# Performance work log

Measured on AMD Instinct MI355X. Metric: run time of the kernel, lower is better.

## Reference

```python
import jax, jax.numpy as jnp
import numpy as np

TAU = 2.0      # LIF membrane time constant
K = 2          # MaxPool1d kernel/stride
ALPHA = 4.0    # spikingjelly surrogate.Sigmoid default alpha
EPS = 1e-5     # BatchNorm1d eps
VTH = 1.0      # LIF v_threshold default

@jax.custom_vjp
def spike(x):
    # Heaviside forward, sigmoid surrogate gradient (spikingjelly surrogate.Sigmoid)
    return (x >= 0.0).astype(x.dtype)

def _spike_fwd(x):
    return spike(x), x

def _spike_bwd(x, g):
    s = jax.nn.sigmoid(ALPHA * x)
    return (g * ALPHA * s * (1.0 - s),)

spike.defvjp(_spike_fwd, _spike_bwd)


def setup_inputs() -> dict:
    key = jax.random.key(0)
    k1, k2 = jax.random.split(key)
    T, B, N, D, O = 4, 32, 1024, 512, 512
    x = jax.random.normal(k1, (T, B, N, D), jnp.float32)
    W = jax.random.normal(k2, (O, D), jnp.float32) * 0.02
    gamma = jnp.ones((O,), jnp.float32)
    beta = jnp.zeros((O,), jnp.float32)
    running_mean = jnp.zeros((O,), jnp.float32)
    running_var = jnp.ones((O,), jnp.float32)
    return {"x": x, "W": W, "gamma": gamma, "beta": beta,
            "running_mean": running_mean, "running_var": running_var}


def reference(x, W, gamma, beta, running_mean, running_var):
    T, B, N, D = x.shape
    O = W.shape[0]
    # Linear (no bias): [T,B,N,D] x [O,D] -> [T,B,N,O]
    h = jnp.einsum('tbnd,od->tbno', x, W)
    # BatchNorm1d in inference form (running stats), fused affine
    inv = gamma * jax.lax.rsqrt(running_var + EPS)
    h = h * inv + (beta - running_mean * inv)
    # MaxPool1d(kernel_size=K, stride=K) over feature dim -> [T,B,N,O//K]
    h = h.reshape(T, B, N, O // K, K).max(axis=-1)
    # Multi-step LIF: v = v + (x - v)/tau; spike = H(v - vth); hard reset to 0
    def step(v, xt):
        v = v + (xt - v) / TAU
        s = spike(v - VTH)
        v = v * (1.0 - jax.lax.stop_gradient(s))  # detach_reset=True
        return v, s
    _, spikes = jax.lax.scan(step, jnp.zeros_like(h[0]), h)
    return spikes
```

## Files before the change

### kernel.cpp

```cpp
#include <hip/hip_runtime.h>

constexpr int T_ = 4, B_ = 32, N_ = 1024, D_ = 512, O_ = 512, OP_ = 256;
constexpr int M_ = T_ * B_ * N_;
constexpr unsigned CAP = 1u * 1024 * 1024;

constexpr size_t WS_CNT  = 0;
constexpr size_t WS_WP   = 1u << 20;
constexpr size_t WS_LIST = WS_WP + (1u << 20);
constexpr size_t WS_NEED = WS_LIST + (size_t)CAP * 4;

constexpr int RSTRIDE = 72;
constexpr int BUFSZ   = 128 * RSTRIDE;

typedef __attribute__((ext_vector_type(8)))  short bf8;
typedef __attribute__((ext_vector_type(16))) float f16v;

union U2B { struct { uint2 a, b; } p; bf8 v; };

__device__ __forceinline__ unsigned cvtpk(float x0, float x1) {
    unsigned r;
    asm("v_cvt_pk_bf16_f32 %0, %1, %2" : "=v"(r) : "v"(x0), "v"(x1));
    return r;
}
__device__ __forceinline__ float hi_lo_f(unsigned u) { return __uint_as_float(u << 16); }
__device__ __forceinline__ float hi_hi_f(unsigned u) { return __uint_as_float(u & 0xffff0000u); }

__global__ __launch_bounds__(256) void k_wprep(const float* __restrict__ W,
                                               unsigned short* __restrict__ wp,
                                               unsigned* __restrict__ cnt)
{
    if (blockIdx.x == 0 && threadIdx.x == 0) *cnt = 0u;
    const int c = blockIdx.x * 256 + threadIdx.x;
    const int lane = c & 63, q = (c >> 6) & 7, j = (c >> 9) & 15, panel = c >> 13;
    const int colblk = panel >> 1, half = panel & 1;
    const int tm = q >> 2, eo = (q >> 1) & 1, Kh = q & 1;
    const int col = colblk * 128 + half * 64 + 2 * (lane & 31) + eo;
    const int k0 = j * 32 + Kh * 16 + (lane >> 5) * 8;
    const float* src = W + (size_t)col * 512 + k0;
    const float4 v0 = *(const float4*)(src);
    const float4 v1 = *(const float4*)(src + 4);
    const float xs[8] = {v0.x, v0.y, v0.z, v0.w, v1.x, v1.y, v1.z, v1.w};
    unsigned o[4];
    #pragma unroll
    for (int p = 0; p < 4; ++p) {
        const unsigned hi = cvtpk(xs[2 * p], xs[2 * p + 1]);
        if (tm == 0) {
            o[p] = hi;
        } else {
            const float l0 = xs[2 * p] - hi_lo_f(hi);
            const float l1 = xs[2 * p + 1] - hi_hi_f(hi);
            o[p] = cvtpk(l0, l1);
        }
    }
    *(uint4*)(wp + (size_t)c * 8) = make_uint4(o[0], o[1], o[2], o[3]);
}

__global__ __launch_bounds__(256, 3) void k_gemm(
    const float* __restrict__ x, const unsigned short* __restrict__ wp,
    const float* __restrict__ gamma, const float* __restrict__ beta,
    const float* __restrict__ rmean, const float* __restrict__ rvar,
    float* __restrict__ out, unsigned* __restrict__ cnt, unsigned* __restrict__ list)
{
    extern __shared__ char lds[];
    const int tid  = threadIdx.x;
    const int lane = tid & 63;
    const int wid  = tid >> 6;

    const int dd = blockIdx.x;
    const int w  = (dd & 7) * 512 + (dd >> 3);
    const int colblk = w & 3, rowblk = w >> 2;
    const int c0  = colblk * 128;
    const int wr0 = (wid >> 1) * 64, wc0 = (wid & 1) * 64;

    const int cE = c0 + wc0 + 2 * (lane & 31);
    const int cO = cE + 1;
    const float invE = gamma[cE] / sqrtf(rvar[cE] + 1e-5f);
    const float addE = beta[cE] - rmean[cE] * invE;
    const float invO = gamma[cO] / sqrtf(rvar[cO] + 1e-5f);
    const float addO = beta[cO] - rmean[cO] * invO;
    asm volatile("s_waitcnt vmcnt(0)" ::: "memory");
    __builtin_amdgcn_sched_barrier(0);

    const int arow = tid >> 1;
    const int kh   = tid & 1;
    const int t_a  = arow & 3;
    const int sl_a = arow >> 2;
    const unsigned vA = (unsigned)(t_a * 32768 + rowblk * 32 + sl_a) * 2048u
                      + (unsigned)kh * 64u;
    const int wA0 = arow * RSTRIDE + kh * 32;

    int rA00, rA01, rA10, rA11;
    {
        const int qv = lane & 31, hs = lane >> 5;
        const int r0 = wr0 + qv, r1 = wr0 + 32 + qv;
        rA00 = r0 * RSTRIDE + 0  + hs * 16;
        rA01 = r0 * RSTRIDE + 32 + hs * 16;
        rA10 = r1 * RSTRIDE + 0  + hs * 16;
        rA11 = r1 * RSTRIDE + 32 + hs * 16;
    }

    const int panel = colblk * 2 + (wid & 1);
    const unsigned vBb = ((unsigned)panel << 17) + (unsigned)lane * 16u;

    f16v accE[2], accO[2];
    #pragma unroll
    for (int i = 0; i < 2; ++i) { accE[i] = (f16v)0.0f; accO[i] = (f16v)0.0f; }

    float4 Aa[4], Ab[4];
    bf8 Bf[8];
    bf8 ah[4];

#define SCHED __builtin_amdgcn_sched_barrier(0)

#define ALOAD(AI, K)                                                              \
    do {                                                                          \
        asm volatile("global_load_dwordx4 %0, %1, %2 offset:%3"                   \
                     : "=v"(AI[0]) : "v"(vA), "s"(x), "n"((K)*128 + 0)  : "memory"); \
        asm volatile("global_load_dwordx4 %0, %1, %2 offset:%3"                   \
                     : "=v"(AI[1]) : "v"(vA), "s"(x), "n"((K)*128 + 16) : "memory"); \
        asm volatile("global_load_dwordx4 %0, %1, %2 offset:%3"                   \
                     : "=v"(AI[2]) : "v"(vA), "s"(x), "n"((K)*128 + 32) : "memory"); \
        asm volatile("global_load_dwordx4 %0, %1, %2 offset:%3"                   \
                     : "=v"(AI[3]) : "v"(vA), "s"(x), "n"((K)*128 + 48) : "memory"); \
    } while (0)

#define BGRP(KH, K)                                                               \
    do {                                                                          \
        const unsigned vk  = vBb + (unsigned)((K) * 8192 + (KH) * 1024);          \
        const unsigned vk2 = vk + 4096u;                                          \
        asm volatile("global_load_dwordx4 %0, %1, %2 offset:%3"                   \
                     : "=v"(Bf[(KH)*4 + 0]) : "v"(vk),  "s"(wp), "n"(0)    : "memory"); \
        asm volatile("global_load_dwordx4 %0, %1, %2 offset:%3"                   \
                     : "=v"(Bf[(KH)*4 + 1]) : "v"(vk),  "s"(wp), "n"(2048) : "memory"); \
        asm volatile("global_load_dwordx4 %0, %1, %2 offset:%3"                   \
                     : "=v"(Bf[(KH)*4 + 2]) : "v"(vk2), "s"(wp), "n"(0)    : "memory"); \
        asm volatile("global_load_dwordx4 %0, %1, %2 offset:%3"                   \
                     : "=v"(Bf[(KH)*4 + 3]) : "v"(vk2), "s"(wp), "n"(2048) : "memory"); \
    } while (0)

#define DSR1(J, IDX, RA)                                                          \
    do {                                                                          \
        const char* bR = lds + ((J) & 1) * BUFSZ;                                 \
        U2B t;                                                                    \
        t.p.a = *(const uint2*)(bR + (RA));                                       \
        t.p.b = *(const uint2*)(bR + (RA) + 8);                                   \
        ah[IDX] = t.v;                                                            \
    } while (0)

#define CONVW(AC, BUF)                                                            \
    do {                                                                          \
        char* pw = lds + (BUF) * BUFSZ + wA0;                                     \
        const unsigned q0 = cvtpk(AC[0].x, AC[0].y), q1 = cvtpk(AC[0].z, AC[0].w);\
        const unsigned q2 = cvtpk(AC[1].x, AC[1].y), q3 = cvtpk(AC[1].z, AC[1].w);\
        *(uint2*)(pw + 0)  = make_uint2(q0, q1);                                  \
        *(uint2*)(pw + 8)  = make_uint2(q2, q3);                                  \
        const unsigned q4 = cvtpk(AC[2].x, AC[2].y), q5 = cvtpk(AC[2].z, AC[2].w);\
        const unsigned q6 = cvtpk(AC[3].x, AC[3].y), q7 = cvtpk(AC[3].z, AC[3].w);\
        *(uint2*)(pw + 16) = make_uint2(q4, q5);                                  \
        *(uint2*)(pw + 24) = make_uint2(q6, q7);                                  \
    } while (0)

#define MGRP4(KH, RT)                                                             \
    do {                                                                          \
        accE[RT] = __builtin_amdgcn_mfma_f32_32x32x16_bf16(ah[(RT)*2+(KH)], Bf[(KH)*4+0], accE[RT], 0, 0, 0); \
        accO[RT] = __builtin_amdgcn_mfma_f32_32x32x16_bf16(ah[(RT)*2+(KH)], Bf[(KH)*4+1], accO[RT], 0, 0, 0); \
        accE[RT] = __builtin_amdgcn_mfma_f32_32x32x16_bf16(ah[(RT)*2+(KH)], Bf[(KH)*4+2], accE[RT], 0, 0, 0); \
        accO[RT] = __builtin_amdgcn_mfma_f32_32x32x16_bf16(ah[(RT)*2+(KH)], Bf[(KH)*4+3], accO[RT], 0, 0, 0); \
    } while (0)

#define PRIO1 __builtin_amdgcn_s_setprio(1)
#define PRIO0 __builtin_amdgcn_s_setprio(0)

#define ITER(J, ATGT, ACV)                                                        \
    do {                                                                          \
        SCHED;                                                                    \
        asm volatile("s_waitcnt vmcnt(8)" ::: "memory");        \
        asm volatile("s_waitcnt lgkmcnt(0)" ::: "memory");      \
        __builtin_amdgcn_s_barrier();                                             \
        SCHED;                                                                    \
        DSR1(J, 0, rA00);                                       \
        SCHED;                                                                    \
        asm volatile("s_waitcnt vmcnt(4)" ::: "memory");       \
        SCHED;                                                                    \
        PRIO1; MGRP4(0, 0); PRIO0;                                                \
        SCHED;                                                                    \
        DSR1(J, 2, rA10);                                       \
        if ((J) + 2 <= 15) { ALOAD(ATGT, (J) + 2); }                              \
        SCHED;                                                                    \
        PRIO1; MGRP4(0, 1); PRIO0;                                                \
        SCHED;                                                                    \
        DSR1(J, 1, rA01);                                       \
        DSR1(J, 3, rA11);                                       \
        BGRP(0, (J) + 1);                                                         \
        SCHED;                                                                    \
        asm volatile("s_waitcnt vmcnt(8)" ::: "memory");       \
        SCHED;                                                                    \
        PRIO1; MGRP4(1, 0); PRIO0;                                                \
        SCHED;                                                                    \
        CONVW(ACV, ((J) + 1) & 1);                             \
        SCHED;                                                                    \
        PRIO1; MGRP4(1, 1); PRIO0;                                                \
        SCHED;                                                                    \
        BGRP(1, (J) + 1);                                                         \
        SCHED;                                                                    \
    } while (0)

    SCHED;
    ALOAD(Aa, 0);
    ALOAD(Ab, 1);
    SCHED;
    BGRP(0, 0);
    BGRP(1, 0);
    SCHED;
    asm volatile("s_waitcnt vmcnt(12)" ::: "memory");
    SCHED;
    CONVW(Aa, 0);
    SCHED;

    ITER(0,  Aa, Ab);
    ITER(1,  Ab, Aa);
    ITER(2,  Aa, Ab);
    ITER(3,  Ab, Aa);
    ITER(4,  Aa, Ab);
    ITER(5,  Ab, Aa);
    ITER(6,  Aa, Ab);
    ITER(7,  Ab, Aa);
    ITER(8,  Aa, Ab);
    ITER(9,  Ab, Aa);
    ITER(10, Aa, Ab);
    ITER(11, Ab, Aa);
    ITER(12, Aa, Ab);
    ITER(13, Ab, Aa);

    SCHED;
    asm volatile("s_waitcnt vmcnt(8)" ::: "memory");
    asm volatile("s_waitcnt lgkmcnt(0)" ::: "memory");
    __builtin_amdgcn_s_barrier();
    SCHED;
    DSR1(14, 0, rA00);
    SCHED;
    asm volatile("s_waitcnt vmcnt(4)" ::: "memory");
    SCHED;
    PRIO1; MGRP4(0, 0); PRIO0;
    SCHED;
    DSR1(14, 2, rA10);
    SCHED;
    PRIO1; MGRP4(0, 1); PRIO0;
    SCHED;
    DSR1(14, 1, rA01);
    DSR1(14, 3, rA11);
    BGRP(0, 15);
    SCHED;
    asm volatile("s_waitcnt vmcnt(4)" ::: "memory");
    SCHED;
    PRIO1; MGRP4(1, 0); PRIO0;
    SCHED;
    CONVW(Ab, 1);
    SCHED;
    PRIO1; MGRP4(1, 1); PRIO0;
    SCHED;
    BGRP(1, 15);
    SCHED;

    asm volatile("s_waitcnt lgkmcnt(0)" ::: "memory");
    __builtin_amdgcn_s_barrier();
    SCHED;
    DSR1(15, 0, rA00);
    DSR1(15, 2, rA10);
    SCHED;
    asm volatile("s_waitcnt vmcnt(4)" ::: "memory");
    SCHED;
    PRIO1; MGRP4(0, 0); PRIO0;
    SCHED;
    DSR1(15, 1, rA01);
    DSR1(15, 3, rA11);
    SCHED;
    PRIO1; MGRP4(0, 1); PRIO0;
    SCHED;
    asm volatile("s_waitcnt vmcnt(0)" ::: "memory");
    SCHED;
    PRIO1; MGRP4(1, 0); PRIO0;
    SCHED;
    PRIO1; MGRP4(1, 1); PRIO0;
    SCHED;

#undef ITER
#undef PRIO1
#undef PRIO0
#undef MGRP4
#undef DSR1
#undef CONVW
#undef BGRP
#undef ALOAD
#undef SCHED

    const int opL = ((c0 + wc0) >> 1) + (lane & 31);
    #pragma unroll
    for (int rt = 0; rt < 2; ++rt) {
        #pragma unroll
        for (int g = 0; g < 4; ++g) {
            const int site = rowblk * 32 + (wid >> 1) * 16 + rt * 8 + 2 * g + (lane >> 5);
            const int bI = site >> 10, nI = site & 1023;
            float v = 0.0f;
            bool flg = false;
            #pragma unroll
            for (int t = 0; t < 4; ++t) {
                const float hE = accE[rt][g * 4 + t] * invE + addE;
                const float hO = accO[rt][g * 4 + t] * invO + addO;
                const float m = fmaxf(hE, hO);
                v = (v + m) * 0.5f;
                const float dv = v - 1.0f;
                const bool sp = dv >= 0.0f;
                out[(((size_t)t * 32 + bI) * 1024 + nI) * 256 + opL] = sp ? 1.0f : 0.0f;
                flg |= (fabsf(dv) < 1e-2f);
                if (sp) v = 0.0f;
            }
            if (flg) {
                unsigned idx = atomicAdd(cnt, 1u);
                if (idx < CAP) list[idx] = ((unsigned)site << 8) | (unsigned)opL;
            }
        }
    }
}

__global__ __launch_bounds__(256) void k_repair(
    const float* __restrict__ x, const float* __restrict__ W,
    const float* __restrict__ gamma, const float* __restrict__ beta,
    const float* __restrict__ rmean, const float* __restrict__ rvar,
    float* __restrict__ out, const unsigned* __restrict__ cnt,
    const unsigned* __restrict__ list)
{
    unsigned count = *cnt;
    if (count > CAP) count = CAP;
    const int lane = threadIdx.x & 63;
    const unsigned gw = (blockIdx.x * 256u + threadIdx.x) >> 6;
    const unsigned nw = (gridDim.x * 256u) >> 6;
    const int d0 = lane * 8;

    for (unsigned j = gw; j < count; j += nw) {
        const unsigned e = list[j];
        const int op = e & 255;
        const int site = e >> 8;
        const int bI = site >> 10, nI = site & 1023;

        double wv[2][8];
        #pragma unroll
        for (int p = 0; p < 2; ++p) {
            const float* Wr = W + (size_t)(2 * op + p) * D_ + d0;
            const float4 a = *(const float4*)(Wr);
            const float4 b = *(const float4*)(Wr + 4);
            wv[p][0] = a.x; wv[p][1] = a.y; wv[p][2] = a.z; wv[p][3] = a.w;
            wv[p][4] = b.x; wv[p][5] = b.y; wv[p][6] = b.z; wv[p][7] = b.w;
        }

        double h[4][2];
        #pragma unroll
        for (int t = 0; t < 4; ++t) {
            const float* xr = x + (((size_t)t * 32 + bI) * 1024 + nI) * D_ + d0;
            const float4 a = *(const float4*)(xr);
            const float4 b = *(const float4*)(xr + 4);
            const double xv[8] = {(double)a.x, (double)a.y, (double)a.z, (double)a.w,
                                  (double)b.x, (double)b.y, (double)b.z, (double)b.w};
            #pragma unroll
            for (int p = 0; p < 2; ++p) {
                double s0 = 0, s1 = 0, s2 = 0, s3 = 0;
                s0 = fma(xv[0], wv[p][0], s0); s1 = fma(xv[1], wv[p][1], s1);
                s2 = fma(xv[2], wv[p][2], s2); s3 = fma(xv[3], wv[p][3], s3);
                s0 = fma(xv[4], wv[p][4], s0); s1 = fma(xv[5], wv[p][5], s1);
                s2 = fma(xv[6], wv[p][6], s2); s3 = fma(xv[7], wv[p][7], s3);
                double s = (s0 + s1) + (s2 + s3);
                #pragma unroll
                for (int off = 32; off > 0; off >>= 1)
                    s += __shfl_xor(s, off, 64);
                h[t][p] = s;
            }
        }

        double iv[2], ad[2];
        #pragma unroll
        for (int p = 0; p < 2; ++p) {
            const int c = 2 * op + p;
            iv[p] = (double)gamma[c] / sqrt((double)rvar[c] + 1e-5);
            ad[p] = (double)beta[c] - (double)rmean[c] * iv[p];
        }
        double v = 0.0;
        #pragma unroll
        for (int t = 0; t < 4; ++t) {
            const double h0 = h[t][0] * iv[0] + ad[0];
            const double h1 = h[t][1] * iv[1] + ad[1];
            const double m = fmax(h0, h1);
            v = (v + m) * 0.5;
            const bool sp = (v >= 1.0);
            if (lane == t)
                out[(((size_t)t * 32 + bI) * 1024 + nI) * 256 + op] = sp ? 1.0f : 0.0f;
            if (sp) v = 0.0;
        }
    }
}

constexpr int FB_SITES = 32, FB_ROWS = 128, FB_BN = 64, FB_BK = 16;

__global__ __launch_bounds__(256)
void snn_fused_f64(const float* __restrict__ x, const float* __restrict__ W,
                   const float* __restrict__ gamma, const float* __restrict__ beta,
                   const float* __restrict__ rmean, const float* __restrict__ rvar,
                   float* __restrict__ out)
{
    __shared__ float As[FB_BK][FB_ROWS];
    __shared__ float Bs[FB_BK][FB_BN];
    const int tid = threadIdx.x;
    const int tx = tid & 15, ty = tid >> 4;
    const int c0 = blockIdx.x * FB_BN;
    const int site_base = blockIdx.y * FB_SITES;
    const int b = site_base / N_, n0 = site_base % N_;
    const int lrow = tid >> 1, lk = (tid & 1) * 8;
    const int s_l = lrow >> 2, t_l = lrow & 3;
    const float* xrow = x + (size_t)((t_l * B_ + b) * N_ + (n0 + s_l)) * D_ + lk;
    const int wc = tid & 63, wk = (tid >> 6) * 4;
    const float* wrow = W + (size_t)(c0 + wc) * D_ + wk;
    double acc[8][4];
    #pragma unroll
    for (int i = 0; i < 8; ++i)
        #pragma unroll
        for (int j = 0; j < 4; ++j) acc[i][j] = 0.0;
    for (int k0 = 0; k0 < D_; k0 += FB_BK) {
        const float4 a0 = *(const float4*)(xrow + k0);
        const float4 a1 = *(const float4*)(xrow + k0 + 4);
        const float4 w4 = *(const float4*)(wrow + k0);
        As[lk + 0][lrow] = a0.x; As[lk + 1][lrow] = a0.y; As[lk + 2][lrow] = a0.z; As[lk + 3][lrow] = a0.w;
        As[lk + 4][lrow] = a1.x; As[lk + 5][lrow] = a1.y; As[lk + 6][lrow] = a1.z; As[lk + 7][lrow] = a1.w;
        Bs[wk + 0][wc] = w4.x; Bs[wk + 1][wc] = w4.y; Bs[wk + 2][wc] = w4.z; Bs[wk + 3][wc] = w4.w;
        __syncthreads();
        #pragma unroll
        for (int k = 0; k < FB_BK; ++k) {
            const float4 af0 = *(const float4*)&As[k][ty * 8];
            const float4 af1 = *(const float4*)&As[k][ty * 8 + 4];
            const float4 bf = *(const float4*)&Bs[k][tx * 4];
            const double ad[8] = {(double)af0.x, (double)af0.y, (double)af0.z, (double)af0.w,
                                  (double)af1.x, (double)af1.y, (double)af1.z, (double)af1.w};
            const double bd[4] = {(double)bf.x, (double)bf.y, (double)bf.z, (double)bf.w};
            #pragma unroll
            for (int i = 0; i < 8; ++i)
                #pragma unroll
                for (int j = 0; j < 4; ++j) acc[i][j] = fma(ad[i], bd[j], acc[i][j]);
        }
        __syncthreads();
    }
    double invd[4], addd[4];
    #pragma unroll
    for (int j = 0; j < 4; ++j) {
        const int c = c0 + tx * 4 + j;
        const double ivv = (double)gamma[c] / sqrt((double)rvar[c] + 1e-5);
        invd[j] = ivv; addd[j] = (double)beta[c] - (double)rmean[c] * ivv;
    }
    #pragma unroll
    for (int si = 0; si < 2; ++si) {
        const int n = n0 + ty * 2 + si;
        #pragma unroll
        for (int p = 0; p < 2; ++p) {
            const int op = (c0 >> 1) + tx * 2 + p;
            double v = 0.0;
            #pragma unroll
            for (int t = 0; t < 4; ++t) {
                const int i = si * 4 + t;
                const double h0 = acc[i][2 * p] * invd[2 * p] + addd[2 * p];
                const double h1 = acc[i][2 * p + 1] * invd[2 * p + 1] + addd[2 * p + 1];
                const double m = fmax(h0, h1);
                v = v + (m - v) * 0.5;
                const bool sp = (v >= 1.0);
                out[((size_t)(t * B_ + b) * N_ + n) * OP_ + op] = sp ? 1.0f : 0.0f;
                if (sp) v = 0.0;
            }
        }
    }
}

extern "C" void kernel_launch(void* const* d_in, const int* in_sizes, int n_in,
                              void* d_out, int out_size, void* d_ws, size_t ws_size,
                              hipStream_t stream)
{
    const float* x     = (const float*)d_in[0];
    const float* W     = (const float*)d_in[1];
    const float* gamma = (const float*)d_in[2];
    const float* beta  = (const float*)d_in[3];
    const float* rmean = (const float*)d_in[4];
    const float* rvar  = (const float*)d_in[5];
    float* out = (float*)d_out;

    if (ws_size < WS_NEED) {
        dim3 grid(O_ / FB_BN, (B_ * N_) / FB_SITES);
        snn_fused_f64<<<grid, dim3(256), 0, stream>>>(x, W, gamma, beta, rmean, rvar, out);
        return;
    }

    char* ws = (char*)d_ws;
    unsigned* cnt = (unsigned*)(ws + WS_CNT);
    unsigned short* wp = (unsigned short*)(ws + WS_WP);
    unsigned* list = (unsigned*)(ws + WS_LIST);

    k_wprep<<<256, 256, 0, stream>>>(W, wp, cnt);
    k_gemm<<<4096, 256, 2 * BUFSZ, stream>>>(x, wp, gamma, beta, rmean, rvar, out, cnt, list);
    k_repair<<<512, 256, 0, stream>>>(x, W, gamma, beta, rmean, rvar, out, cnt, list);
}
```

Measured before the change: 201.7 us.

## Drop split-bf16 weight residual term, halving MFMA work; widen repair band

The weight prep no longer emits a bf16 hi/lo split. The GEMM now issues half as many MFMAs and B-operand loads per k-step, using single-bf16 weights, and the inner loop schedule is restructured to match. To make up for the lost precision, the near-threshold flag band that routes outputs to the exact fp32/f64 repair kernel is widened from 1e-2 to 2.5e-2, so more sites may need repair. The aim is to cut matrix-core and weight-load cost in the main kernel, at the price of more repair work and a correctness risk if bf16-weight errors ever exceed the band.

```diff
diff --git a/kernel.cpp b/kernel.cpp
--- a/kernel.cpp
+++ b/kernel.cpp
@@ -6,7 +6,7 @@
 
 constexpr size_t WS_CNT  = 0;
 constexpr size_t WS_WP   = 1u << 20;
-constexpr size_t WS_LIST = WS_WP + (1u << 20);
+constexpr size_t WS_LIST = WS_WP + (1u << 19);
 constexpr size_t WS_NEED = WS_LIST + (size_t)CAP * 4;
 
 constexpr int RSTRIDE = 72;
@@ -22,8 +22,6 @@
     asm("v_cvt_pk_bf16_f32 %0, %1, %2" : "=v"(r) : "v"(x0), "v"(x1));
     return r;
 }
-__device__ __forceinline__ float hi_lo_f(unsigned u) { return __uint_as_float(u << 16); }
-__device__ __forceinline__ float hi_hi_f(unsigned u) { return __uint_as_float(u & 0xffff0000u); }
 
 __global__ __launch_bounds__(256) void k_wprep(const float* __restrict__ W,
                                                unsigned short* __restrict__ wp,
@@ -31,28 +29,17 @@
 {
     if (blockIdx.x == 0 && threadIdx.x == 0) *cnt = 0u;
     const int c = blockIdx.x * 256 + threadIdx.x;
-    const int lane = c & 63, q = (c >> 6) & 7, j = (c >> 9) & 15, panel = c >> 13;
+    const int lane = c & 63, q = (c >> 6) & 3, j = (c >> 8) & 15, panel = c >> 12;
     const int colblk = panel >> 1, half = panel & 1;
-    const int tm = q >> 2, eo = (q >> 1) & 1, Kh = q & 1;
+    const int eo = (q >> 1) & 1, Kh = q & 1;
     const int col = colblk * 128 + half * 64 + 2 * (lane & 31) + eo;
     const int k0 = j * 32 + Kh * 16 + (lane >> 5) * 8;
     const float* src = W + (size_t)col * 512 + k0;
     const float4 v0 = *(const float4*)(src);
     const float4 v1 = *(const float4*)(src + 4);
-    const float xs[8] = {v0.x, v0.y, v0.z, v0.w, v1.x, v1.y, v1.z, v1.w};
-    unsigned o[4];
-    #pragma unroll
-    for (int p = 0; p < 4; ++p) {
-        const unsigned hi = cvtpk(xs[2 * p], xs[2 * p + 1]);
-        if (tm == 0) {
-            o[p] = hi;
-        } else {
-            const float l0 = xs[2 * p] - hi_lo_f(hi);
-            const float l1 = xs[2 * p + 1] - hi_hi_f(hi);
-            o[p] = cvtpk(l0, l1);
-        }
-    }
-    *(uint4*)(wp + (size_t)c * 8) = make_uint4(o[0], o[1], o[2], o[3]);
+    const unsigned o0 = cvtpk(v0.x, v0.y), o1 = cvtpk(v0.z, v0.w);
+    const unsigned o2 = cvtpk(v1.x, v1.y), o3 = cvtpk(v1.z, v1.w);
+    *(uint4*)(wp + (size_t)c * 8) = make_uint4(o0, o1, o2, o3);
 }
 
 __global__ __launch_bounds__(256, 3) void k_gemm(
@@ -100,14 +87,14 @@
     }
 
     const int panel = colblk * 2 + (wid & 1);
-    const unsigned vBb = ((unsigned)panel << 17) + (unsigned)lane * 16u;
+    const unsigned vBb = ((unsigned)panel << 16) + (unsigned)lane * 16u;
 
     f16v accE[2], accO[2];
     #pragma unroll
     for (int i = 0; i < 2; ++i) { accE[i] = (f16v)0.0f; accO[i] = (f16v)0.0f; }
 
     float4 Aa[4], Ab[4];
-    bf8 Bf[8];
+    bf8 Bf[4];
     bf8 ah[4];
 
 #define SCHED __builtin_amdgcn_sched_barrier(0)
@@ -124,18 +111,15 @@
                      : "=v"(AI[3]) : "v"(vA), "s"(x), "n"((K)*128 + 48) : "memory"); \
     } while (0)
 
-#define BGRP(KH, K)                                                               \
-    do {                                                                          \
-        const unsigned vk  = vBb + (unsigned)((K) * 8192 + (KH) * 1024);          \
-        const unsigned vk2 = vk + 4096u;                                          \
-        asm volatile("global_load_dwordx4 %0, %1, %2 offset:%3"                   \
-                     : "=v"(Bf[(KH)*4 + 0]) : "v"(vk),  "s"(wp), "n"(0)    : "memory"); \
-        asm volatile("global_load_dwordx4 %0, %1, %2 offset:%3"                   \
-                     : "=v"(Bf[(KH)*4 + 1]) : "v"(vk),  "s"(wp), "n"(2048) : "memory"); \
-        asm volatile("global_load_dwordx4 %0, %1, %2 offset:%3"                   \
-                     : "=v"(Bf[(KH)*4 + 2]) : "v"(vk2), "s"(wp), "n"(0)    : "memory"); \
-        asm volatile("global_load_dwordx4 %0, %1, %2 offset:%3"                   \
-                     : "=v"(Bf[(KH)*4 + 3]) : "v"(vk2), "s"(wp), "n"(2048) : "memory"); \
+#define BGRPH(KH, K)                                                              \
+    do {                                                                          \
+        const unsigned vk = vBb + (unsigned)(K) * 4096u;                          \
+        asm volatile("global_load_dwordx4 %0, %1, %2 offset:%3"                   \
+                     : "=v"(Bf[0 + (KH)]) : "v"(vk), "s"(wp),                     \
+                       "n"((KH)*1024)        : "memory");                         \
+        asm volatile("global_load_dwordx4 %0, %1, %2 offset:%3"                   \
+                     : "=v"(Bf[2 + (KH)]) : "v"(vk), "s"(wp),                     \
+                       "n"(2048 + (KH)*1024) : "memory");                         \
     } while (0)
 
 #define DSR1(J, IDX, RA)                                                          \
@@ -160,48 +144,45 @@
         *(uint2*)(pw + 24) = make_uint2(q6, q7);                                  \
     } while (0)
 
-#define MGRP4(KH, RT)                                                             \
-    do {                                                                          \
-        accE[RT] = __builtin_amdgcn_mfma_f32_32x32x16_bf16(ah[(RT)*2+(KH)], Bf[(KH)*4+0], accE[RT], 0, 0, 0); \
-        accO[RT] = __builtin_amdgcn_mfma_f32_32x32x16_bf16(ah[(RT)*2+(KH)], Bf[(KH)*4+1], accO[RT], 0, 0, 0); \
-        accE[RT] = __builtin_amdgcn_mfma_f32_32x32x16_bf16(ah[(RT)*2+(KH)], Bf[(KH)*4+2], accE[RT], 0, 0, 0); \
-        accO[RT] = __builtin_amdgcn_mfma_f32_32x32x16_bf16(ah[(RT)*2+(KH)], Bf[(KH)*4+3], accO[RT], 0, 0, 0); \
+#define MGRP(KH)                                                                  \
+    do {                                                                          \
+        accE[0] = __builtin_amdgcn_mfma_f32_32x32x16_bf16(ah[0 + (KH)], Bf[0 + (KH)], accE[0], 0, 0, 0); \
+        accO[0] = __builtin_amdgcn_mfma_f32_32x32x16_bf16(ah[0 + (KH)], Bf[2 + (KH)], accO[0], 0, 0, 0); \
+        accE[1] = __builtin_amdgcn_mfma_f32_32x32x16_bf16(ah[2 + (KH)], Bf[0 + (KH)], accE[1], 0, 0, 0); \
+        accO[1] = __builtin_amdgcn_mfma_f32_32x32x16_bf16(ah[2 + (KH)], Bf[2 + (KH)], accO[1], 0, 0, 0); \
     } while (0)
 
 #define PRIO1 __builtin_amdgcn_s_setprio(1)
 #define PRIO0 __builtin_amdgcn_s_setprio(0)
 
-#define ITER(J, ATGT, ACV)                                                        \
-    do {                                                                          \
-        SCHED;                                                                    \
-        asm volatile("s_waitcnt vmcnt(8)" ::: "memory");        \
+#define ITER(J, ATGT, ACV, NB0, NB1)                                              \
+    do {                                                                          \
+        SCHED;                                                                    \
+        asm volatile("s_waitcnt vmcnt(4)" ::: "memory");        \
         asm volatile("s_waitcnt lgkmcnt(0)" ::: "memory");      \
         __builtin_amdgcn_s_barrier();                                             \
         SCHED;                                                                    \
-        DSR1(J, 0, rA00);                                       \
-        SCHED;                                                                    \
-        asm volatile("s_waitcnt vmcnt(4)" ::: "memory");       \
-        SCHED;                                                                    \
-        PRIO1; MGRP4(0, 0); PRIO0;                                                \
-        SCHED;                                                                    \
-        DSR1(J, 2, rA10);                                       \
+        DSR1(J, 0, rA00);                                                         \
+        DSR1(J, 1, rA01);                                                         \
+        DSR1(J, 2, rA10);                                                         \
+        DSR1(J, 3, rA11);                                                         \
+        SCHED;                                                                    \
         if ((J) + 2 <= 15) { ALOAD(ATGT, (J) + 2); }                              \
         SCHED;                                                                    \
-        PRIO1; MGRP4(0, 1); PRIO0;                                                \
-        SCHED;                                                                    \
-        DSR1(J, 1, rA01);                                       \
-        DSR1(J, 3, rA11);                                       \
-        BGRP(0, (J) + 1);                                                         \
-        SCHED;                                                                    \
-        asm volatile("s_waitcnt vmcnt(8)" ::: "memory");       \
-        SCHED;                                                                    \
-        PRIO1; MGRP4(1, 0); PRIO0;                                                \
+        asm volatile("s_waitcnt vmcnt(" NB0 ")" ::: "memory");   \
+        asm volatile("s_waitcnt lgkmcnt(0)" ::: "memory");     \
+        SCHED;                                                                    \
+        PRIO1; MGRP(0); PRIO0;                                                    \
+        SCHED;                                                                    \
+        BGRPH(0, (J) + 1);                                                        \
+        SCHED;                                                                    \
+        asm volatile("s_waitcnt vmcnt(" NB1 ")" ::: "memory");   \
+        SCHED;                                                                    \
+        PRIO1; MGRP(1); PRIO0;                                                    \
         SCHED;                                                                    \
         CONVW(ACV, ((J) + 1) & 1);                             \
         SCHED;                                                                    \
-        PRIO1; MGRP4(1, 1); PRIO0;                                                \
-        SCHED;                                                                    \
-        BGRP(1, (J) + 1);                                                         \
+        BGRPH(1, (J) + 1);                                                        \
         SCHED;                                                                    \
     } while (0)
 
@@ -209,88 +190,56 @@
     ALOAD(Aa, 0);
     ALOAD(Ab, 1);
     SCHED;
-    BGRP(0, 0);
-    BGRP(1, 0);
-    SCHED;
-    asm volatile("s_waitcnt vmcnt(12)" ::: "memory");
+    BGRPH(0, 0);
+    BGRPH(1, 0);
+    SCHED;
+    asm volatile("s_waitcnt vmcnt(8)" ::: "memory");
     SCHED;
     CONVW(Aa, 0);
     SCHED;
 
-    ITER(0,  Aa, Ab);
-    ITER(1,  Ab, Aa);
-    ITER(2,  Aa, Ab);
-    ITER(3,  Ab, Aa);
-    ITER(4,  Aa, Ab);
-    ITER(5,  Ab, Aa);
-    ITER(6,  Aa, Ab);
-    ITER(7,  Ab, Aa);
-    ITER(8,  Aa, Ab);
-    ITER(9,  Ab, Aa);
-    ITER(10, Aa, Ab);
-    ITER(11, Ab, Aa);
-    ITER(12, Aa, Ab);
-    ITER(13, Ab, Aa);
-
-    SCHED;
-    asm volatile("s_waitcnt vmcnt(8)" ::: "memory");
+    ITER(0,  Aa, Ab, "6", "6");
+    ITER(1,  Ab, Aa, "6", "6");
+    ITER(2,  Aa, Ab, "6", "6");
+    ITER(3,  Ab, Aa, "6", "6");
+    ITER(4,  Aa, Ab, "6", "6");
+    ITER(5,  Ab, Aa, "6", "6");
+    ITER(6,  Aa, Ab, "6", "6");
+    ITER(7,  Ab, Aa, "6", "6");
+    ITER(8,  Aa, Ab, "6", "6");
+    ITER(9,  Ab, Aa, "6", "6");
+    ITER(10, Aa, Ab, "6", "6");
+    ITER(11, Ab, Aa, "6", "6");
+    ITER(12, Aa, Ab, "6", "6");
+    ITER(13, Ab, Aa, "6", "6");
+    ITER(14, Aa, Ab, "2", "2");
+
+    SCHED;
     asm volatile("s_waitcnt lgkmcnt(0)" ::: "memory");
     __builtin_amdgcn_s_barrier();
     SCHED;
-    DSR1(14, 0, rA00);
-    SCHED;
-    asm volatile("s_waitcnt vmcnt(4)" ::: "memory");
-    SCHED;
-    PRIO1; MGRP4(0, 0); PRIO0;
-    SCHED;
-    DSR1(14, 2, rA10);
-    SCHED;
-    PRIO1; MGRP4(0, 1); PRIO0;
-    SCHED;
-    DSR1(14, 1, rA01);
-    DSR1(14, 3, rA11);
-    BGRP(0, 15);
-    SCHED;
-    asm volatile("s_waitcnt vmcnt(4)" ::: "memory");
-    SCHED;
-    PRIO1; MGRP4(1, 0); PRIO0;
-    SCHED;
-    CONVW(Ab, 1);
-    SCHED;
-    PRIO1; MGRP4(1, 1); PRIO0;
-    SCHED;
-    BGRP(1, 15);
-    SCHED;
-
+    DSR1(15, 0, rA00);
+    DSR1(15, 1, rA01);
+    DSR1(15, 2, rA10);
+    DSR1(15, 3, rA11);
+    SCHED;
+    asm volatile("s_waitcnt vmcnt(2)" ::: "memory");
     asm volatile("s_waitcnt lgkmcnt(0)" ::: "memory");
-    __builtin_amdgcn_s_barrier();
-    SCHED;
-    DSR1(15, 0, rA00);
-    DSR1(15, 2, rA10);
-    SCHED;
-    asm volatile("s_waitcnt vmcnt(4)" ::: "memory");
-    SCHED;
-    PRIO1; MGRP4(0, 0); PRIO0;
-    SCHED;
-    DSR1(15, 1, rA01);
-    DSR1(15, 3, rA11);
-    SCHED;
-    PRIO1; MGRP4(0, 1); PRIO0;
+    SCHED;
+    PRIO1; MGRP(0); PRIO0;
     SCHED;
     asm volatile("s_waitcnt vmcnt(0)" ::: "memory");
     SCHED;
-    PRIO1; MGRP4(1, 0); PRIO0;
-    SCHED;
-    PRIO1; MGRP4(1, 1); PRIO0;
+    PRIO1; MGRP(1); PRIO0;
     SCHED;
 
 #undef ITER
 #undef PRIO1
 #undef PRIO0
-#undef MGRP4
+#undef MGRP
 #undef DSR1
 #undef CONVW
-#undef BGRP
+#undef BGRPH
 #undef ALOAD
 #undef SCHED
 
@@ -312,7 +261,7 @@
                 const float dv = v - 1.0f;
                 const bool sp = dv >= 0.0f;
                 out[(((size_t)t * 32 + bI) * 1024 + nI) * 256 + opL] = sp ? 1.0f : 0.0f;
-                flg |= (fabsf(dv) < 1e-2f);
+                flg |= (fabsf(dv) < 2.5e-2f);
                 if (sp) v = 0.0f;
             }
             if (flg) {
@@ -498,7 +447,7 @@
     unsigned short* wp = (unsigned short*)(ws + WS_WP);
     unsigned* list = (unsigned*)(ws + WS_LIST);
 
-    k_wprep<<<256, 256, 0, stream>>>(W, wp, cnt);
+    k_wprep<<<128, 256, 0, stream>>>(W, wp, cnt);
     k_gemm<<<4096, 256, 2 * BUFSZ, stream>>>(x, wp, gamma, beta, rmean, rvar, out, cnt, list);
     k_repair<<<512, 256, 0, stream>>>(x, W, gamma, beta, rmean, rvar, out, cnt, list);
 }
```

Measured after the change: 175.7 us (median of 2 runs). -12.9%, faster.
